# Optimization experiments

Measured on AMD Instinct MI355X. Metric: run time of the kernel, lower is better.

## Reference

```python
import jax, jax.numpy as jnp
import numpy as np

B, C, H, W = 4, 128, 128, 128
G, K = 4, 3
P = K * K
STRIDE, PAD, DIL = 1, 1, 1
OFFSET_SCALE = 1.0


def setup_inputs() -> dict:
    key = jax.random.key(0)
    k1, k2, k3, k4 = jax.random.split(key, 4)
    inp = jax.random.normal(k1, (B, C, H, W), jnp.float32)
    # offset / mask linear params (zero-init in source; small random here for a
    # nontrivial sampling pattern -- same math, different param values)
    W_off = jax.random.normal(k2, (C, G * P * 2), jnp.float32) * 0.01
    b_off = jax.random.normal(k3, (G * P * 2,), jnp.float32) * 0.5
    W_mask = jax.random.normal(k4, (C, G * P), jnp.float32) * 0.02
    b_mask = jnp.zeros((G * P,), jnp.float32)
    return {"inp": inp, "W_off": W_off, "b_off": b_off, "W_mask": W_mask, "b_mask": b_mask}


def _dcnv3_core(x, offset, mask):
    # x: (b,h,w,c)  offset: (b,h,w,G*P*2)  mask: (b,h,w,G*P)
    b, h, w, c = x.shape
    gc = c // G
    xp = jnp.pad(x, ((0, 0), (PAD, PAD), (PAD, PAD), (0, 0)))
    H_in, W_in = h + 2 * PAD, w + 2 * PAD
    H_out = (H_in - (DIL * (K - 1) + 1)) // STRIDE + 1
    W_out = (W_in - (DIL * (K - 1) + 1)) // STRIDE + 1
    Q = H_out * W_out

    # reference points, normalized to padded size (matches _get_reference_points)
    base = (DIL * (K - 1)) // 2 + 0.5
    ref_y = (base + jnp.arange(H_out, dtype=jnp.float32) * STRIDE) / H_in
    ref_x = (base + jnp.arange(W_out, dtype=jnp.float32) * STRIDE) / W_in
    ref = jnp.stack(jnp.broadcast_arrays(ref_x[None, :], ref_y[:, None]), -1)  # (Ho,Wo,2) as (x,y)

    # dilation grid (matches _generate_dilation_grids; torch meshgrid flatten is x-major)
    off0 = -((DIL * (K - 1)) // 2)
    ks = off0 + jnp.arange(K, dtype=jnp.float32) * DIL
    gx = jnp.repeat(ks, K) / W_in  # (P,)
    gy = jnp.tile(ks, K) / H_in
    grid = jnp.stack([gx, gy], -1)  # (P,2), identical for every group

    norm = jnp.array([W_in, H_in], jnp.float32)
    loc = (ref[None, :, :, None, None, :]
           + grid[None, None, None, None, :, :] * OFFSET_SCALE
           + offset.reshape(b, H_out, W_out, G, P, 2) * (OFFSET_SCALE / norm))  # (b,Ho,Wo,G,P,2)

    # grid_sample(bilinear, zeros, align_corners=False): pixel = loc*size - 0.5
    px = loc[..., 0] * W_in - 0.5
    py = loc[..., 1] * H_in - 0.5
    x0 = jnp.floor(px); y0 = jnp.floor(py)
    tx = px - x0; ty = py - y0
    x0i = x0.astype(jnp.int32); y0i = y0.astype(jnp.int32)

    xg = xp.reshape(b, H_in * W_in, G, gc)

    def corner(ix, iy, wgt):
        valid = (ix >= 0) & (ix < W_in) & (iy >= 0) & (iy < H_in)
        lin = jnp.clip(iy, 0, H_in - 1) * W_in + jnp.clip(ix, 0, W_in - 1)
        idx = lin.reshape(b, Q, G, P).transpose(0, 1, 3, 2).reshape(b, Q * P, G)
        g = jnp.take_along_axis(xg, idx[..., None], axis=1)  # (b,Q*P,G,gc)
        wv = jnp.where(valid, wgt, 0.0).reshape(b, Q, G, P).transpose(0, 1, 3, 2).reshape(b, Q * P, G, 1)
        return g * wv

    val = (corner(x0i, y0i, (1 - tx) * (1 - ty))
           + corner(x0i + 1, y0i, tx * (1 - ty))
           + corner(x0i, y0i + 1, (1 - tx) * ty)
           + corner(x0i + 1, y0i + 1, tx * ty))  # (b,Q*P,G,gc)

    m = mask.reshape(b, Q, G, P).transpose(0, 1, 3, 2).reshape(b, Q, P, G, 1)
    out = (val.reshape(b, Q, P, G, gc) * m).sum(axis=2)  # (b,Q,G,gc)
    return out.reshape(b, H_out, W_out, G * gc)


def reference(inp, W_off, b_off, W_mask, b_mask):
    b, c, h, w = inp.shape
    x = inp.reshape(b, h, w, c)  # torch .view reinterpretation (faithful to source)
    offset = x @ W_off + b_off  # (b,h,w,G*P*2)
    mask = jax.nn.softmax((x @ W_mask + b_mask).reshape(b, h, w, G, P), axis=-1).reshape(b, h, w, G * P)
    out = _dcnv3_core(x, offset, mask)  # (b,h,w,c)
    return out.reshape(b, c, h, w)
```

## Files before the change

### kernel.cpp

```cpp
#include <hip/hip_runtime.h>


#define NPIX 65536

typedef unsigned int uint;
typedef unsigned short ushort;
typedef __attribute__((ext_vector_type(8))) short short8v;
typedef __attribute__((ext_vector_type(4))) float f32x4;

__device__ __forceinline__ ushort f2bf(float f) {
  uint u = __float_as_uint(f);
  u += 0x7FFFu + ((u >> 16) & 1u);
  return (ushort)(u >> 16);
}
__device__ __forceinline__ uint pkbf(float lo, float hi) {
  return (uint)f2bf(lo) | ((uint)f2bf(hi) << 16);
}
__device__ __forceinline__ float bflo(uint d) { return __uint_as_float(d << 16); }
__device__ __forceinline__ float bfhi(uint d) { return __uint_as_float(d & 0xFFFF0000u); }
__device__ __forceinline__ ushort f2h(float f) {
  union { _Float16 h; ushort u; } cv;
  cv.h = (_Float16)f;
  return cv.u;
}
__device__ __forceinline__ float h2f_lo(uint u) {
  union { ushort s; _Float16 h; } cv;
  cv.s = (ushort)(u & 0xFFFFu);
  return (float)cv.h;
}
__device__ __forceinline__ float h2f_hi(uint u) {
  union { ushort s; _Float16 h; } cv;
  cv.s = (ushort)(u >> 16);
  return (float)cv.h;
}

union U8 { uint u[4]; short8v v; };

__global__ __launch_bounds__(256) void dcn_lin_mfma(
    const float* __restrict__ x, const float* __restrict__ Woff,
    const float* __restrict__ boff, const float* __restrict__ Wmask,
    const float* __restrict__ bmask, ushort* __restrict__ ws16,
    ushort* __restrict__ x16) {
  __shared__ uint wt[112 * 68];
  __shared__ float bias_lds[112];
  const int pbase = blockIdx.x << 6;
  const int t = threadIdx.x;

  {
    int n = t, row = 0;
    bool act = true;
    if (t >= 224) act = false;
    else if (t >= 112) { n = t - 112; row = 1; }
    if (act) {
      for (int kp = row; kp < 64; kp += 2) {
        const int k = kp << 1;
        float w0, w1;
        if (n < 72) {
          w0 = Woff[k * 72 + n];        w1 = Woff[k * 72 + 72 + n];
        } else if (n < 108) {
          w0 = Wmask[k * 36 + n - 72];  w1 = Wmask[k * 36 + 36 + n - 72];
        } else {
          w0 = 0.f; w1 = 0.f;
        }
        wt[n * 68 + kp] = pkbf(w0, w1);
      }
    }
    if (t < 112)
      bias_lds[t] = (t < 72) ? boff[t] : (t < 108 ? bmask[t - 72] : 0.f);
  }

  if (x16) {
    const int pix2 = pbase + (t >> 2);
    const int quad = t & 3;
    const float* xp = x + (size_t)pix2 * 128 + (quad << 5);
    const int bb = pix2 >> 14, yx = pix2 & 16383;
    ushort* dst = x16 + ((((size_t)((quad << 2) | bb) << 14) | yx) << 5);
#pragma unroll
    for (int ck = 0; ck < 2; ++ck) {
      const float4 a = *(const float4*)(xp + ck * 16);
      const float4 b4 = *(const float4*)(xp + ck * 16 + 4);
      const float4 c4 = *(const float4*)(xp + ck * 16 + 8);
      const float4 d4 = *(const float4*)(xp + ck * 16 + 12);
      uint4 s0, s1;
      s0.x = pkbf(a.x, a.y);   s0.y = pkbf(a.z, a.w);
      s0.z = pkbf(b4.x, b4.y); s0.w = pkbf(b4.z, b4.w);
      s1.x = pkbf(c4.x, c4.y); s1.y = pkbf(c4.z, c4.w);
      s1.z = pkbf(d4.x, d4.y); s1.w = pkbf(d4.z, d4.w);
      *(uint4*)(dst + ck * 16) = s0;
      *(uint4*)(dst + ck * 16 + 8) = s1;
    }
  }
  __syncthreads();

  const int wv = t >> 6;
  const int lane = t & 63;
  const int lrow = lane & 15;
  const int lhi = lane >> 4;
  const int pixrow = pbase + (wv << 4) + lrow;

  U8 afr[4];
#pragma unroll
  for (int kt = 0; kt < 4; ++kt) {
    const float* ax = x + (size_t)pixrow * 128 + (kt << 5) + (lhi << 3);
    const float4 xa = *(const float4*)ax;
    const float4 xb4 = *(const float4*)(ax + 4);
    afr[kt].u[0] = pkbf(xa.x, xa.y);   afr[kt].u[1] = pkbf(xa.z, xa.w);
    afr[kt].u[2] = pkbf(xb4.x, xb4.y); afr[kt].u[3] = pkbf(xb4.z, xb4.w);
  }

  f32x4 acc[7];
#pragma unroll
  for (int nt = 0; nt < 7; ++nt) {
    const float bv = bias_lds[(nt << 4) + lrow];
    f32x4 a4 = {bv, bv, bv, bv};
#pragma unroll
    for (int kt = 0; kt < 4; ++kt) {
      U8 bfr;
      const uint4 bw =
          *(const uint4*)(wt + ((nt << 4) + lrow) * 68 + (kt << 4) + (lhi << 2));
      bfr.u[0] = bw.x; bfr.u[1] = bw.y; bfr.u[2] = bw.z; bfr.u[3] = bw.w;
      a4 = __builtin_amdgcn_mfma_f32_16x16x32_bf16(afr[kt].v, bfr.v, a4, 0, 0, 0);
    }
    acc[nt] = a4;
  }

  __syncthreads();
  {
    ushort* tl = (ushort*)wt;
    const int plb = (wv << 4) + (lhi << 2);
#pragma unroll
    for (int nt = 0; nt < 7; ++nt) {
      const int n = (nt << 4) + lrow;
      if (n < 108) {
        int ridx;
        if (n < 72) {
          const int gg = n / 18;
          ridx = (gg << 5) + (n - gg * 18);
        } else {
          const int m = n - 72;
          const int gg = m / 9;
          ridx = (gg << 5) + 18 + (m - gg * 9);
        }
        tl[(plb + 0) * 128 + ridx] = f2h(acc[nt].x);
        tl[(plb + 1) * 128 + ridx] = f2h(acc[nt].y);
        tl[(plb + 2) * 128 + ridx] = f2h(acc[nt].z);
        tl[(plb + 3) * 128 + ridx] = f2h(acc[nt].w);
      }
    }
  }
  __syncthreads();
  {
    const uint* src = (const uint*)wt;
    uint4* dst = (uint4*)(ws16 + (size_t)pbase * 128);
#pragma unroll
    for (int i = 0; i < 4; ++i) {
      const int idx = (i << 8) + t;
      const uint4 v = *(const uint4*)(src + idx * 4);
      dst[idx] = v;
    }
  }
}

__global__ __launch_bounds__(256) void dcn_samp(
    const ushort* __restrict__ x16, const ushort* __restrict__ ws16,
    float* __restrict__ out) {
  const int g = blockIdx.x & 3;
  const int pg = threadIdx.x >> 2;
  const int sub = threadIdx.x & 3;
  const int q = ((blockIdx.x >> 2) << 6) | pg;
  const int b = q >> 14;
  const int h = (q >> 7) & 127;
  const int w = q & 127;
  const ushort* xg = x16 + (((size_t)((g << 2) | b)) << 19) + (sub << 3);

  const ushort* wsrec = ws16 + (size_t)q * 128 + (g << 5);
  const uint4 r0 = *(const uint4*)(wsrec);
  const uint4 r1 = *(const uint4*)(wsrec + 8);
  const uint4 r2 = *(const uint4*)(wsrec + 16);
  const uint2 r3 = *(const uint2*)(wsrec + 24);
  const uint rr0 = r0.x, rr1 = r0.y, rr2 = r0.z, rr3 = r0.w;
  const uint rr4 = r1.x, rr5 = r1.y, rr6 = r1.z, rr7 = r1.w;
  const uint rr8 = r2.x, rr9 = r2.y, rr10 = r2.z, rr11 = r2.w;
  const uint rr12 = r3.x, rr13 = r3.y;

  float offx9[9], offy9[9], mk9[9];
  {
    const uint rra[14] = {rr0, rr1, rr2,  rr3,  rr4,  rr5,  rr6,
                          rr7, rr8, rr9, rr10, rr11, rr12, rr13};
#pragma unroll
    for (int p = 0; p < 9; ++p) {
      offx9[p] = h2f_lo(rra[p]);
      offy9[p] = h2f_hi(rra[p]);
      const int li = 18 + p;
      mk9[p] = (li & 1) ? h2f_hi(rra[li >> 1]) : h2f_lo(rra[li >> 1]);
    }
    float mx = mk9[0];
#pragma unroll
    for (int p = 1; p < 9; ++p) mx = fmaxf(mx, mk9[p]);
    float s = 0.f;
#pragma unroll
    for (int p = 0; p < 9; ++p) {
      mk9[p] = __expf(mk9[p] - mx);
      s += mk9[p];
    }
    const float sinv = 1.0f / s;
#pragma unroll
    for (int p = 0; p < 9; ++p) mk9[p] *= sinv;
  }

  float a0 = 0.f, a1 = 0.f, a2 = 0.f, a3 = 0.f;
  float a4 = 0.f, a5 = 0.f, a6 = 0.f, a7 = 0.f;

#pragma unroll
  for (int p = 0; p < 9; ++p) {
    const float mk = mk9[p];
    const float px = (float)(w + p / 3) + offx9[p];
    const float py = (float)(h + p % 3) + offy9[p];
    const float fx = floorf(px), fy = floorf(py);
    const float tx = px - fx, ty = py - fy;
    const int x0 = (int)fx - 1, y0 = (int)fy - 1;
    const int x1 = x0 + 1, y1 = y0 + 1;
    const float ax0 = ((unsigned)x0 < 128u) ? (1.f - tx) : 0.f;
    const float ax1 = ((unsigned)x1 < 128u) ? tx : 0.f;
    const float ay0 = ((unsigned)y0 < 128u) ? (mk * (1.f - ty)) : 0.f;
    const float ay1 = ((unsigned)y1 < 128u) ? (mk * ty) : 0.f;
    const float w00 = ax0 * ay0, w10 = ax1 * ay0;
    const float w01 = ax0 * ay1, w11 = ax1 * ay1;
    const int cx0 = min(max(x0, 0), 127), cy0 = min(max(y0, 0), 127);
    const int cx1 = min(max(x1, 0), 127), cy1 = min(max(y1, 0), 127);
    const int o00 = ((cy0 << 7) | cx0) << 5;
    const int o10 = ((cy0 << 7) | cx1) << 5;
    const int o01 = ((cy1 << 7) | cx0) << 5;
    const int o11 = ((cy1 << 7) | cx1) << 5;
    const uint4 d00 = *(const uint4*)(xg + o00);
    const uint4 d10 = *(const uint4*)(xg + o10);
    const uint4 d01 = *(const uint4*)(xg + o01);
    const uint4 d11 = *(const uint4*)(xg + o11);
    a0 = fmaf(w00, bflo(d00.x), fmaf(w10, bflo(d10.x),
         fmaf(w01, bflo(d01.x), fmaf(w11, bflo(d11.x), a0))));
    a1 = fmaf(w00, bfhi(d00.x), fmaf(w10, bfhi(d10.x),
         fmaf(w01, bfhi(d01.x), fmaf(w11, bfhi(d11.x), a1))));
    a2 = fmaf(w00, bflo(d00.y), fmaf(w10, bflo(d10.y),
         fmaf(w01, bflo(d01.y), fmaf(w11, bflo(d11.y), a2))));
    a3 = fmaf(w00, bfhi(d00.y), fmaf(w10, bfhi(d10.y),
         fmaf(w01, bfhi(d01.y), fmaf(w11, bfhi(d11.y), a3))));
    a4 = fmaf(w00, bflo(d00.z), fmaf(w10, bflo(d10.z),
         fmaf(w01, bflo(d01.z), fmaf(w11, bflo(d11.z), a4))));
    a5 = fmaf(w00, bfhi(d00.z), fmaf(w10, bfhi(d10.z),
         fmaf(w01, bfhi(d01.z), fmaf(w11, bfhi(d11.z), a5))));
    a6 = fmaf(w00, bflo(d00.w), fmaf(w10, bflo(d10.w),
         fmaf(w01, bflo(d01.w), fmaf(w11, bflo(d11.w), a6))));
    a7 = fmaf(w00, bfhi(d00.w), fmaf(w10, bfhi(d10.w),
         fmaf(w01, bfhi(d01.w), fmaf(w11, bfhi(d11.w), a7))));
  }

  float* op = out + (size_t)q * 128 + (g << 5) + (sub << 3);
  float4 oa, ob;
  oa.x = a0; oa.y = a1; oa.z = a2; oa.w = a3;
  ob.x = a4; ob.y = a5; ob.z = a6; ob.w = a7;
  *(float4*)op = oa;
  *(float4*)(op + 4) = ob;
}

__global__ __launch_bounds__(256) void dcn_lin(
    const float* __restrict__ x, const float* __restrict__ Woff,
    const float* __restrict__ boff, const float* __restrict__ Wmask,
    const float* __restrict__ bmask, float* __restrict__ ws) {
  const int jg = blockIdx.x >> 8;
  const int pix = ((blockIdx.x & 255) << 8) | threadIdx.x;
  const float* W;
  const float* bias;
  int ldw, obase;
  if (jg == 0) {
    W = Woff; bias = boff; ldw = 72; obase = 0;
  } else if (jg == 1) {
    W = Woff + 36; bias = boff + 36; ldw = 72; obase = 36;
  } else {
    W = Wmask; bias = bmask; ldw = 36; obase = 72;
  }
  float acc[36];
#pragma unroll
  for (int j = 0; j < 36; ++j) acc[j] = bias[j];
  const float* xp = x + (size_t)pix * 128;
  for (int c0 = 0; c0 < 128; c0 += 8) {
    float xr[8];
    *(float4*)(xr) = *(const float4*)(xp + c0);
    *(float4*)(xr + 4) = *(const float4*)(xp + c0 + 4);
#pragma unroll
    for (int cc = 0; cc < 8; ++cc) {
      const float xc = xr[cc];
      const float* wr = W + (size_t)(c0 + cc) * ldw;
#pragma unroll
      for (int j = 0; j < 36; ++j) acc[j] = fmaf(xc, wr[j], acc[j]);
    }
  }
  if (jg == 2) {
#pragma unroll
    for (int g = 0; g < 4; ++g) {
      float mx = acc[g * 9];
#pragma unroll
      for (int p = 1; p < 9; ++p) mx = fmaxf(mx, acc[g * 9 + p]);
      float s = 0.f;
#pragma unroll
      for (int p = 0; p < 9; ++p) {
        acc[g * 9 + p] = __expf(acc[g * 9 + p] - mx);
        s += acc[g * 9 + p];
      }
      const float sinv = 1.0f / s;
#pragma unroll
      for (int p = 0; p < 9; ++p) acc[g * 9 + p] *= sinv;
    }
  }
#pragma unroll
  for (int j = 0; j < 36; ++j) ws[(size_t)(obase + j) * NPIX + pix] = acc[j];
}

__global__ __launch_bounds__(256) void dcn_samp_f32(
    const float* __restrict__ x, const float* __restrict__ ws,
    float* __restrict__ out) {
  const int q = (blockIdx.x << 4) | (threadIdx.x >> 4);
  const int sub = threadIdx.x & 15;
  const int c = sub << 3;
  const int g = sub >> 2;
  const int b = q >> 14;
  const int h = (q >> 7) & 127;
  const int w = q & 127;
  const float* xb = x + ((size_t)b << 21) + c;
  const float* wsq = ws + q;
  float a0 = 0.f, a1 = 0.f, a2 = 0.f, a3 = 0.f;
  float a4 = 0.f, a5 = 0.f, a6 = 0.f, a7 = 0.f;
#pragma unroll
  for (int p = 0; p < 9; ++p) {
    const float offx = wsq[(size_t)(g * 18 + p * 2) * NPIX];
    const float offy = wsq[(size_t)(g * 18 + p * 2 + 1) * NPIX];
    const float mk = wsq[(size_t)(72 + g * 9 + p) * NPIX];
    const float px = (float)(w + p / 3) + offx;
    const float py = (float)(h + p % 3) + offy;
    const float fx = floorf(px), fy = floorf(py);
    const float tx = px - fx, ty = py - fy;
    const int x0 = (int)fx - 1, y0 = (int)fy - 1;
    const int x1 = x0 + 1, y1 = y0 + 1;
    const float ax0 = ((unsigned)x0 < 128u) ? (1.f - tx) : 0.f;
    const float ax1 = ((unsigned)x1 < 128u) ? tx : 0.f;
    const float ay0 = ((unsigned)y0 < 128u) ? (mk * (1.f - ty)) : 0.f;
    const float ay1 = ((unsigned)y1 < 128u) ? (mk * ty) : 0.f;
    const float w00 = ax0 * ay0, w10 = ax1 * ay0;
    const float w01 = ax0 * ay1, w11 = ax1 * ay1;
    const int cx0 = min(max(x0, 0), 127), cy0 = min(max(y0, 0), 127);
    const int cx1 = min(max(x1, 0), 127), cy1 = min(max(y1, 0), 127);
    const int o00 = (cy0 << 14) | (cx0 << 7), o10 = (cy0 << 14) | (cx1 << 7);
    const int o01 = (cy1 << 14) | (cx0 << 7), o11 = (cy1 << 14) | (cx1 << 7);
    const float4 v00a = *(const float4*)(xb + o00);
    const float4 v00b = *(const float4*)(xb + o00 + 4);
    const float4 v10a = *(const float4*)(xb + o10);
    const float4 v10b = *(const float4*)(xb + o10 + 4);
    const float4 v01a = *(const float4*)(xb + o01);
    const float4 v01b = *(const float4*)(xb + o01 + 4);
    const float4 v11a = *(const float4*)(xb + o11);
    const float4 v11b = *(const float4*)(xb + o11 + 4);
    a0 = fmaf(w00, v00a.x, fmaf(w10, v10a.x, fmaf(w01, v01a.x, fmaf(w11, v11a.x, a0))));
    a1 = fmaf(w00, v00a.y, fmaf(w10, v10a.y, fmaf(w01, v01a.y, fmaf(w11, v11a.y, a1))));
    a2 = fmaf(w00, v00a.z, fmaf(w10, v10a.z, fmaf(w01, v01a.z, fmaf(w11, v11a.z, a2))));
    a3 = fmaf(w00, v00a.w, fmaf(w10, v10a.w, fmaf(w01, v01a.w, fmaf(w11, v11a.w, a3))));
    a4 = fmaf(w00, v00b.x, fmaf(w10, v10b.x, fmaf(w01, v01b.x, fmaf(w11, v11b.x, a4))));
    a5 = fmaf(w00, v00b.y, fmaf(w10, v10b.y, fmaf(w01, v01b.y, fmaf(w11, v11b.y, a5))));
    a6 = fmaf(w00, v00b.z, fmaf(w10, v10b.z, fmaf(w01, v01b.z, fmaf(w11, v11b.z, a6))));
    a7 = fmaf(w00, v00b.w, fmaf(w10, v10b.w, fmaf(w01, v01b.w, fmaf(w11, v11b.w, a7))));
  }
  float4 oa, ob;
  oa.x = a0; oa.y = a1; oa.z = a2; oa.w = a3;
  ob.x = a4; ob.y = a5; ob.z = a6; ob.w = a7;
  float* op = out + (size_t)q * 128 + c;
  *(float4*)op = oa;
  *(float4*)(op + 4) = ob;
}

__global__ __launch_bounds__(128) void dcn_fused(
    const float* __restrict__ x, const float* __restrict__ Woff,
    const float* __restrict__ boff, const float* __restrict__ Wmask,
    const float* __restrict__ bmask, float* __restrict__ out) {
  __shared__ float xs[128];
  __shared__ float res[108];
  __shared__ float msk[36];
  const int q = blockIdx.x;
  const int t = threadIdx.x;
  const int b = q >> 14, h = (q >> 7) & 127, w = q & 127;
  xs[t] = x[(size_t)q * 128 + t];
  __syncthreads();
  if (t < 108) {
    float a;
    const float* W;
    int ld;
    if (t < 72) {
      a = boff[t]; W = Woff + t; ld = 72;
    } else {
      a = bmask[t - 72]; W = Wmask + (t - 72); ld = 36;
    }
    for (int cc = 0; cc < 128; ++cc) a = fmaf(xs[cc], W[(size_t)cc * ld], a);
    res[t] = a;
  }
  __syncthreads();
  if (t < 4) {
    float mx = -1e30f;
    for (int p = 0; p < 9; ++p) mx = fmaxf(mx, res[72 + t * 9 + p]);
    float s = 0.f;
    float e[9];
    for (int p = 0; p < 9; ++p) {
      e[p] = __expf(res[72 + t * 9 + p] - mx);
      s += e[p];
    }
    for (int p = 0; p < 9; ++p) msk[t * 9 + p] = e[p] / s;
  }
  __syncthreads();
  const int g = t >> 5;
  const float* xb = x + ((size_t)b << 21) + t;
  float acc = 0.f;
#pragma unroll
  for (int p = 0; p < 9; ++p) {
    const float offx = res[g * 18 + p * 2];
    const float offy = res[g * 18 + p * 2 + 1];
    const float px = (float)(w + p / 3) + offx;
    const float py = (float)(h + p % 3) + offy;
    const float fx = floorf(px), fy = floorf(py);
    const float tx = px - fx, ty = py - fy;
    const int x0 = (int)fx - 1, y0 = (int)fy - 1;
    float sv = 0.f;
#define CORNER1(XI, YI, WT)                                       \
  if ((unsigned)(XI) < 128u && (unsigned)(YI) < 128u)             \
    sv = fmaf((WT), xb[((size_t)(YI) << 14) + ((size_t)(XI) << 7)], sv);
    CORNER1(x0, y0, (1.f - tx) * (1.f - ty))
    CORNER1(x0 + 1, y0, tx * (1.f - ty))
    CORNER1(x0, y0 + 1, (1.f - tx) * ty)
    CORNER1(x0 + 1, y0 + 1, tx * ty)
#undef CORNER1
    acc = fmaf(msk[g * 9 + p], sv, acc);
  }
  out[(size_t)q * 128 + t] = acc;
}

extern "C" void kernel_launch(void* const* d_in, const int* in_sizes, int n_in,
                              void* d_out, int out_size, void* d_ws,
                              size_t ws_size, hipStream_t stream) {
  const float* x = (const float*)d_in[0];
  const float* Woff = (const float*)d_in[1];
  const float* boff = (const float*)d_in[2];
  const float* Wmask = (const float*)d_in[3];
  const float* bmask = (const float*)d_in[4];
  float* out = (float*)d_out;
  const size_t need_ws = (size_t)NPIX * 108 * sizeof(float);
  const size_t need_full = (size_t)NPIX * (128 + 128) * sizeof(ushort);
  if (ws_size >= need_full) {
    ushort* x16 = (ushort*)d_ws;
    ushort* ws16 = (ushort*)d_ws + (size_t)NPIX * 128;
    dcn_lin_mfma<<<1024, 256, 0, stream>>>(x, Woff, boff, Wmask, bmask, ws16,
                                           x16);
    dcn_samp<<<4096, 256, 0, stream>>>(x16, ws16, out);
  } else if (ws_size >= need_ws) {
    float* ws = (float*)d_ws;
    dcn_lin<<<768, 256, 0, stream>>>(x, Woff, boff, Wmask, bmask, ws);
    dcn_samp_f32<<<4096, 256, 0, stream>>>(x, ws, out);
  } else {
    dcn_fused<<<NPIX, 128, 0, stream>>>(x, Woff, boff, Wmask, bmask, out);
  }
}
```

Baseline: 60.87 us.

## Fuse offset/mask projection into sampling kernel via per-group MFMA

```diff
diff --git a/kernel.cpp b/kernel.cpp
--- a/kernel.cpp
+++ b/kernel.cpp
@@ -36,44 +36,25 @@
 
 union U8 { uint u[4]; short8v v; };
 
-__global__ __launch_bounds__(256) void dcn_lin_mfma(
+__device__ __forceinline__ float wcol(const float* __restrict__ Woff,
+                                      const float* __restrict__ Wmask,
+                                      int g, int k, int n) {
+  if (n < 18) return Woff[k * 72 + g * 18 + n];
+  if (n < 27) return Wmask[k * 36 + g * 9 + (n - 18)];
+  return 0.f;
+}
+
+__global__ __launch_bounds__(256) void dcn_pack(
     const float* __restrict__ x, const float* __restrict__ Woff,
     const float* __restrict__ boff, const float* __restrict__ Wmask,
-    const float* __restrict__ bmask, ushort* __restrict__ ws16,
-    ushort* __restrict__ x16) {
-  __shared__ uint wt[112 * 68];
-  __shared__ float bias_lds[112];
-  const int pbase = blockIdx.x << 6;
+    const float* __restrict__ bmask, ushort* __restrict__ x16,
+    uint* __restrict__ wpk, float* __restrict__ wb) {
   const int t = threadIdx.x;
-
-  {
-    int n = t, row = 0;
-    bool act = true;
-    if (t >= 224) act = false;
-    else if (t >= 112) { n = t - 112; row = 1; }
-    if (act) {
-      for (int kp = row; kp < 64; kp += 2) {
-        const int k = kp << 1;
-        float w0, w1;
-        if (n < 72) {
-          w0 = Woff[k * 72 + n];        w1 = Woff[k * 72 + 72 + n];
-        } else if (n < 108) {
-          w0 = Wmask[k * 36 + n - 72];  w1 = Wmask[k * 36 + 36 + n - 72];
-        } else {
-          w0 = 0.f; w1 = 0.f;
-        }
-        wt[n * 68 + kp] = pkbf(w0, w1);
-      }
-    }
-    if (t < 112)
-      bias_lds[t] = (t < 72) ? boff[t] : (t < 108 ? bmask[t - 72] : 0.f);
-  }
-
-  if (x16) {
-    const int pix2 = pbase + (t >> 2);
+  if (blockIdx.x < 1024) {
+    const int pix = (blockIdx.x << 6) + (t >> 2);
     const int quad = t & 3;
-    const float* xp = x + (size_t)pix2 * 128 + (quad << 5);
-    const int bb = pix2 >> 14, yx = pix2 & 16383;
+    const float* xp = x + (size_t)pix * 128 + (quad << 5);
+    const int bb = pix >> 14, yx = pix & 16383;
     ushort* dst = x16 + ((((size_t)((quad << 2) | bb) << 14) | yx) << 5);
 #pragma unroll
     for (int ck = 0; ck < 2; ++ck) {
@@ -89,91 +70,86 @@
       *(uint4*)(dst + ck * 16) = s0;
       *(uint4*)(dst + ck * 16 + 8) = s1;
     }
+  } else {
+    for (int i = 0; i < 32; ++i) {
+      const int idx = (i << 8) + t;
+      const int f = idx >> 8;
+      const int widx = idx & 255;
+      const int lane = widx >> 2;
+      const int epair = widx & 3;
+      const int kt = f & 3;
+      const int nt = (f >> 2) & 1;
+      const int g = f >> 3;
+      const int k0 = kt * 32 + (lane >> 4) * 8 + epair * 2;
+      const int n = nt * 16 + (lane & 15);
+      const float w0 = wcol(Woff, Wmask, g, k0, n);
+      const float w1 = wcol(Woff, Wmask, g, k0 + 1, n);
+      wpk[idx] = pkbf(w0, w1);
+    }
+    if (t < 128) {
+      const int g = t >> 5, n = t & 31;
+      float bv;
+      if (n < 18) bv = boff[g * 18 + n];
+      else if (n < 27) bv = bmask[g * 9 + (n - 18)];
+      else bv = 0.f;
+      wb[t] = bv;
+    }
+  }
+}
+
+__global__ __launch_bounds__(256) void dcn_fsamp(
+    const ushort* __restrict__ x16, const uint* __restrict__ wpk,
+    const float* __restrict__ wb, float* __restrict__ out) {
+  __shared__ __align__(16) ushort rec[64 * 40];
+  const int g = blockIdx.x & 3;
+  const int pbase = (blockIdx.x >> 2) << 6;
+  const int t = threadIdx.x;
+  const int b = pbase >> 14;
+
+  {
+    const int wv = t >> 6;
+    const int lane = t & 63;
+    const int lrow = lane & 15;
+    const int lhi = lane >> 4;
+    const int yx = (pbase + (wv << 4) + lrow) & 16383;
+
+    const float bv0 = wb[(g << 5) + lrow];
+    const float bv1 = wb[(g << 5) + 16 + lrow];
+    f32x4 acc0 = {bv0, bv0, bv0, bv0};
+    f32x4 acc1 = {bv1, bv1, bv1, bv1};
+
+#pragma unroll
+    for (int kt = 0; kt < 4; ++kt) {
+      U8 a, b0, b1;
+      const uint4 av = *(const uint4*)(
+          x16 + ((((size_t)((kt << 2) | b) << 14) | yx) << 5) + (lhi << 3));
+      a.u[0] = av.x; a.u[1] = av.y; a.u[2] = av.z; a.u[3] = av.w;
+      const uint4 b0v = *(const uint4*)(wpk + (g * 8 + kt) * 256 + (lane << 2));
+      b0.u[0] = b0v.x; b0.u[1] = b0v.y; b0.u[2] = b0v.z; b0.u[3] = b0v.w;
+      const uint4 b1v =
+          *(const uint4*)(wpk + (g * 8 + 4 + kt) * 256 + (lane << 2));
+      b1.u[0] = b1v.x; b1.u[1] = b1v.y; b1.u[2] = b1v.z; b1.u[3] = b1v.w;
+      acc0 = __builtin_amdgcn_mfma_f32_16x16x32_bf16(a.v, b0.v, acc0, 0, 0, 0);
+      acc1 = __builtin_amdgcn_mfma_f32_16x16x32_bf16(a.v, b1.v, acc1, 0, 0, 0);
+    }
+
+    const int px0 = (wv << 4) + (lhi << 2);
+#pragma unroll
+    for (int j = 0; j < 4; ++j) {
+      rec[(px0 + j) * 40 + lrow] = f2h(acc0[j]);
+      rec[(px0 + j) * 40 + 16 + lrow] = f2h(acc1[j]);
+    }
   }
   __syncthreads();
 
-  const int wv = t >> 6;
-  const int lane = t & 63;
-  const int lrow = lane & 15;
-  const int lhi = lane >> 4;
-  const int pixrow = pbase + (wv << 4) + lrow;
-
-  U8 afr[4];
-#pragma unroll
-  for (int kt = 0; kt < 4; ++kt) {
-    const float* ax = x + (size_t)pixrow * 128 + (kt << 5) + (lhi << 3);
-    const float4 xa = *(const float4*)ax;
-    const float4 xb4 = *(const float4*)(ax + 4);
-    afr[kt].u[0] = pkbf(xa.x, xa.y);   afr[kt].u[1] = pkbf(xa.z, xa.w);
-    afr[kt].u[2] = pkbf(xb4.x, xb4.y); afr[kt].u[3] = pkbf(xb4.z, xb4.w);
-  }
-
-  f32x4 acc[7];
-#pragma unroll
-  for (int nt = 0; nt < 7; ++nt) {
-    const float bv = bias_lds[(nt << 4) + lrow];
-    f32x4 a4 = {bv, bv, bv, bv};
-#pragma unroll
-    for (int kt = 0; kt < 4; ++kt) {
-      U8 bfr;
-      const uint4 bw =
-          *(const uint4*)(wt + ((nt << 4) + lrow) * 68 + (kt << 4) + (lhi << 2));
-      bfr.u[0] = bw.x; bfr.u[1] = bw.y; bfr.u[2] = bw.z; bfr.u[3] = bw.w;
-      a4 = __builtin_amdgcn_mfma_f32_16x16x32_bf16(afr[kt].v, bfr.v, a4, 0, 0, 0);
-    }
-    acc[nt] = a4;
-  }
-
-  __syncthreads();
-  {
-    ushort* tl = (ushort*)wt;
-    const int plb = (wv << 4) + (lhi << 2);
-#pragma unroll
-    for (int nt = 0; nt < 7; ++nt) {
-      const int n = (nt << 4) + lrow;
-      if (n < 108) {
-        int ridx;
-        if (n < 72) {
-          const int gg = n / 18;
-          ridx = (gg << 5) + (n - gg * 18);
-        } else {
-          const int m = n - 72;
-          const int gg = m / 9;
-          ridx = (gg << 5) + 18 + (m - gg * 9);
-        }
-        tl[(plb + 0) * 128 + ridx] = f2h(acc[nt].x);
-        tl[(plb + 1) * 128 + ridx] = f2h(acc[nt].y);
-        tl[(plb + 2) * 128 + ridx] = f2h(acc[nt].z);
-        tl[(plb + 3) * 128 + ridx] = f2h(acc[nt].w);
-      }
-    }
-  }
-  __syncthreads();
-  {
-    const uint* src = (const uint*)wt;
-    uint4* dst = (uint4*)(ws16 + (size_t)pbase * 128);
-#pragma unroll
-    for (int i = 0; i < 4; ++i) {
-      const int idx = (i << 8) + t;
-      const uint4 v = *(const uint4*)(src + idx * 4);
-      dst[idx] = v;
-    }
-  }
-}
-
-__global__ __launch_bounds__(256) void dcn_samp(
-    const ushort* __restrict__ x16, const ushort* __restrict__ ws16,
-    float* __restrict__ out) {
-  const int g = blockIdx.x & 3;
-  const int pg = threadIdx.x >> 2;
-  const int sub = threadIdx.x & 3;
-  const int q = ((blockIdx.x >> 2) << 6) | pg;
-  const int b = q >> 14;
+  const int pg = t >> 2;
+  const int sub = t & 3;
+  const int q = pbase + pg;
   const int h = (q >> 7) & 127;
   const int w = q & 127;
   const ushort* xg = x16 + (((size_t)((g << 2) | b)) << 19) + (sub << 3);
 
-  const ushort* wsrec = ws16 + (size_t)q * 128 + (g << 5);
+  const ushort* wsrec = rec + pg * 40;
   const uint4 r0 = *(const uint4*)(wsrec);
   const uint4 r1 = *(const uint4*)(wsrec + 8);
   const uint4 r2 = *(const uint4*)(wsrec + 16);
@@ -447,14 +423,17 @@
   const float* Wmask = (const float*)d_in[3];
   const float* bmask = (const float*)d_in[4];
   float* out = (float*)d_out;
+  const size_t x16_bytes = (size_t)NPIX * 128 * sizeof(ushort);
+  const size_t wpk_bytes = 8192 * sizeof(uint);
+  const size_t need_full = x16_bytes + wpk_bytes + 128 * sizeof(float);
   const size_t need_ws = (size_t)NPIX * 108 * sizeof(float);
-  const size_t need_full = (size_t)NPIX * (128 + 128) * sizeof(ushort);
   if (ws_size >= need_full) {
     ushort* x16 = (ushort*)d_ws;
-    ushort* ws16 = (ushort*)d_ws + (size_t)NPIX * 128;
-    dcn_lin_mfma<<<1024, 256, 0, stream>>>(x, Woff, boff, Wmask, bmask, ws16,
-                                           x16);
-    dcn_samp<<<4096, 256, 0, stream>>>(x16, ws16, out);
+    uint* wpk = (uint*)((char*)d_ws + x16_bytes);
+    float* wb = (float*)((char*)d_ws + x16_bytes + wpk_bytes);
+    dcn_pack<<<1025, 256, 0, stream>>>(x, Woff, boff, Wmask, bmask, x16, wpk,
+                                       wb);
+    dcn_fsamp<<<4096, 256, 0, stream>>>(x16, wpk, wb, out);
   } else if (ws_size >= need_ws) {
     float* ws = (float*)d_ws;
     dcn_lin<<<768, 256, 0, stream>>>(x, Woff, boff, Wmask, bmask, ws);
```

New measurement: 74.53 us. 1.22x slower.

## Prepack projection weights into MFMA fragment layout in a separate kernel

Applied to the files above, without the earlier changes.

```diff
diff --git a/kernel.cpp b/kernel.cpp
--- a/kernel.cpp
+++ b/kernel.cpp
@@ -36,40 +36,47 @@
 
 union U8 { uint u[4]; short8v v; };
 
-__global__ __launch_bounds__(256) void dcn_lin_mfma(
-    const float* __restrict__ x, const float* __restrict__ Woff,
-    const float* __restrict__ boff, const float* __restrict__ Wmask,
-    const float* __restrict__ bmask, ushort* __restrict__ ws16,
+__device__ __forceinline__ float wcol(const float* __restrict__ Woff,
+                                      const float* __restrict__ Wmask,
+                                      int g, int k, int n) {
+  if (n < 18) return Woff[k * 72 + g * 18 + n];
+  if (n < 27) return Wmask[k * 36 + g * 9 + (n - 18)];
+  return 0.f;
+}
+
+__global__ __launch_bounds__(256) void dcn_wpack(
+    const float* __restrict__ Woff, const float* __restrict__ boff,
+    const float* __restrict__ Wmask, const float* __restrict__ bmask,
+    uint* __restrict__ wpk, float* __restrict__ wb) {
+  const int idx = (blockIdx.x << 8) + threadIdx.x;
+  {
+    const int f = idx >> 8;
+    const int widx = idx & 255;
+    const int lane = widx >> 2, epair = widx & 3;
+    const int kt = f & 3, nt = (f >> 2) & 1, g = f >> 3;
+    const int k0 = kt * 32 + (lane >> 4) * 8 + epair * 2;
+    const int n = nt * 16 + (lane & 15);
+    wpk[idx] = pkbf(wcol(Woff, Wmask, g, k0, n), wcol(Woff, Wmask, g, k0 + 1, n));
+  }
+  if (blockIdx.x == 0 && threadIdx.x < 128) {
+    const int g = threadIdx.x >> 5, n = threadIdx.x & 31;
+    float bv;
+    if (n < 18) bv = boff[g * 18 + n];
+    else if (n < 27) bv = bmask[g * 9 + (n - 18)];
+    else bv = 0.f;
+    wb[threadIdx.x] = bv;
+  }
+}
+
+__global__ __launch_bounds__(256) void dcn_lin2(
+    const float* __restrict__ x, const uint* __restrict__ wpk,
+    const float* __restrict__ wb, ushort* __restrict__ ws16,
     ushort* __restrict__ x16) {
-  __shared__ uint wt[112 * 68];
-  __shared__ float bias_lds[112];
+  __shared__ __align__(16) ushort rec[64 * 136];
   const int pbase = blockIdx.x << 6;
   const int t = threadIdx.x;
 
   {
-    int n = t, row = 0;
-    bool act = true;
-    if (t >= 224) act = false;
-    else if (t >= 112) { n = t - 112; row = 1; }
-    if (act) {
-      for (int kp = row; kp < 64; kp += 2) {
-        const int k = kp << 1;
-        float w0, w1;
-        if (n < 72) {
-          w0 = Woff[k * 72 + n];        w1 = Woff[k * 72 + 72 + n];
-        } else if (n < 108) {
-          w0 = Wmask[k * 36 + n - 72];  w1 = Wmask[k * 36 + 36 + n - 72];
-        } else {
-          w0 = 0.f; w1 = 0.f;
-        }
-        wt[n * 68 + kp] = pkbf(w0, w1);
-      }
-    }
-    if (t < 112)
-      bias_lds[t] = (t < 72) ? boff[t] : (t < 108 ? bmask[t - 72] : 0.f);
-  }
-
-  if (x16) {
     const int pix2 = pbase + (t >> 2);
     const int quad = t & 3;
     const float* xp = x + (size_t)pix2 * 128 + (quad << 5);
@@ -90,7 +97,6 @@
       *(uint4*)(dst + ck * 16 + 8) = s1;
     }
   }
-  __syncthreads();
 
   const int wv = t >> 6;
   const int lane = t & 63;
@@ -108,55 +114,50 @@
     afr[kt].u[2] = pkbf(xb4.x, xb4.y); afr[kt].u[3] = pkbf(xb4.z, xb4.w);
   }
 
-  f32x4 acc[7];
-#pragma unroll
-  for (int nt = 0; nt < 7; ++nt) {
-    const float bv = bias_lds[(nt << 4) + lrow];
-    f32x4 a4 = {bv, bv, bv, bv};
-#pragma unroll
-    for (int kt = 0; kt < 4; ++kt) {
-      U8 bfr;
-      const uint4 bw =
-          *(const uint4*)(wt + ((nt << 4) + lrow) * 68 + (kt << 4) + (lhi << 2));
-      bfr.u[0] = bw.x; bfr.u[1] = bw.y; bfr.u[2] = bw.z; bfr.u[3] = bw.w;
-      a4 = __builtin_amdgcn_mfma_f32_16x16x32_bf16(afr[kt].v, bfr.v, a4, 0, 0, 0);
-    }
-    acc[nt] = a4;
-  }
-
+  f32x4 acc[4][2];
+#pragma unroll
+  for (int g = 0; g < 4; ++g)
+#pragma unroll
+    for (int nt = 0; nt < 2; ++nt) {
+      const float bv = wb[(g << 5) + (nt << 4) + lrow];
+      acc[g][nt] = (f32x4){bv, bv, bv, bv};
+    }
+
+#pragma unroll
+  for (int kt = 0; kt < 4; ++kt)
+#pragma unroll
+    for (int g = 0; g < 4; ++g)
+#pragma unroll
+      for (int nt = 0; nt < 2; ++nt) {
+        U8 bf;
+        const uint4 bv =
+            *(const uint4*)(wpk + ((g << 3) + (nt << 2) + kt) * 256 + (lane << 2));
+        bf.u[0] = bv.x; bf.u[1] = bv.y; bf.u[2] = bv.z; bf.u[3] = bv.w;
+        acc[g][nt] =
+            __builtin_amdgcn_mfma_f32_16x16x32_bf16(afr[kt].v, bf.v, acc[g][nt], 0, 0, 0);
+      }
+
+  {
+    const int px0 = (wv << 4) + (lhi << 2);
+#pragma unroll
+    for (int g = 0; g < 4; ++g)
+#pragma unroll
+      for (int nt = 0; nt < 2; ++nt)
+#pragma unroll
+        for (int j = 0; j < 4; ++j)
+          rec[(px0 + j) * 136 + (g << 5) + (nt << 4) + lrow] = f2h(acc[g][nt][j]);
+  }
   __syncthreads();
+
   {
-    ushort* tl = (ushort*)wt;
-    const int plb = (wv << 4) + (lhi << 2);
-#pragma unroll
-    for (int nt = 0; nt < 7; ++nt) {
-      const int n = (nt << 4) + lrow;
-      if (n < 108) {
-        int ridx;
-        if (n < 72) {
-          const int gg = n / 18;
-          ridx = (gg << 5) + (n - gg * 18);
-        } else {
-          const int m = n - 72;
-          const int gg = m / 9;
-          ridx = (gg << 5) + 18 + (m - gg * 9);
-        }
-        tl[(plb + 0) * 128 + ridx] = f2h(acc[nt].x);
-        tl[(plb + 1) * 128 + ridx] = f2h(acc[nt].y);
-        tl[(plb + 2) * 128 + ridx] = f2h(acc[nt].z);
-        tl[(plb + 3) * 128 + ridx] = f2h(acc[nt].w);
-      }
-    }
-  }
-  __syncthreads();
-  {
-    const uint* src = (const uint*)wt;
-    uint4* dst = (uint4*)(ws16 + (size_t)pbase * 128);
+    ushort* dst = ws16 + (size_t)pbase * 128;
 #pragma unroll
     for (int i = 0; i < 4; ++i) {
       const int idx = (i << 8) + t;
-      const uint4 v = *(const uint4*)(src + idx * 4);
-      dst[idx] = v;
+      const int px = idx >> 4;
+      const int col = (idx & 15) << 3;
+      const uint4 v = *(const uint4*)(rec + px * 136 + col);
+      *(uint4*)(dst + (size_t)idx * 8) = v;
     }
   }
 }
@@ -447,13 +448,18 @@
   const float* Wmask = (const float*)d_in[3];
   const float* bmask = (const float*)d_in[4];
   float* out = (float*)d_out;
+  const size_t x16_bytes = (size_t)NPIX * 128 * sizeof(ushort);
+  const size_t ws16_bytes = (size_t)NPIX * 128 * sizeof(ushort);
+  const size_t wpk_bytes = 8192 * sizeof(uint);
+  const size_t need_full = x16_bytes + ws16_bytes + wpk_bytes + 512;
   const size_t need_ws = (size_t)NPIX * 108 * sizeof(float);
-  const size_t need_full = (size_t)NPIX * (128 + 128) * sizeof(ushort);
   if (ws_size >= need_full) {
     ushort* x16 = (ushort*)d_ws;
-    ushort* ws16 = (ushort*)d_ws + (size_t)NPIX * 128;
-    dcn_lin_mfma<<<1024, 256, 0, stream>>>(x, Woff, boff, Wmask, bmask, ws16,
-                                           x16);
+    ushort* ws16 = (ushort*)((char*)d_ws + x16_bytes);
+    uint* wpk = (uint*)((char*)d_ws + x16_bytes + ws16_bytes);
+    float* wb = (float*)((char*)d_ws + x16_bytes + ws16_bytes + wpk_bytes);
+    dcn_wpack<<<32, 256, 0, stream>>>(Woff, boff, Wmask, bmask, wpk, wb);
+    dcn_lin2<<<1024, 256, 0, stream>>>(x, wpk, wb, ws16, x16);
     dcn_samp<<<4096, 256, 0, stream>>>(x16, ws16, out);
   } else if (ws_size >= need_ws) {
     float* ws = (float*)d_ws;
```

New measurement: 61.92 us. No clear change (+1.7%).
